# Kernel optimization log

Hardware: AMD Instinct MI355X
Metric: run time of the kernel (lower is better)

## Reference

```python
import jax, jax.numpy as jnp
import numpy as np

N = 100000
E = 625000
IN_C, HID_C, OUT_C = 128, 128, 128


def setup_inputs() -> dict:
    key = jax.random.key(0)
    ks = jax.random.split(key, 8)
    x = jax.random.normal(ks[0], (N, IN_C), dtype=jnp.float32)
    edge_index = jax.random.randint(ks[1], (2, E), 0, N, dtype=jnp.int64)
    # SAGEConv layer 1: lin_l (on aggregated neighbors, with bias), lin_r (on root, no bias)
    s1 = 1.0 / np.sqrt(IN_C)
    W1l = jax.random.uniform(ks[2], (HID_C, IN_C), minval=-s1, maxval=s1, dtype=jnp.float32)
    b1l = jax.random.uniform(ks[3], (HID_C,), minval=-s1, maxval=s1, dtype=jnp.float32)
    W1r = jax.random.uniform(ks[4], (HID_C, IN_C), minval=-s1, maxval=s1, dtype=jnp.float32)
    s2 = 1.0 / np.sqrt(HID_C)
    W2l = jax.random.uniform(ks[5], (OUT_C, HID_C), minval=-s2, maxval=s2, dtype=jnp.float32)
    b2l = jax.random.uniform(ks[6], (OUT_C,), minval=-s2, maxval=s2, dtype=jnp.float32)
    W2r = jax.random.uniform(ks[7], (OUT_C, HID_C), minval=-s2, maxval=s2, dtype=jnp.float32)
    return {"x": x, "edge_index": edge_index,
            "W1l": W1l, "b1l": b1l, "W1r": W1r,
            "W2l": W2l, "b2l": b2l, "W2r": W2r}


def _sage_conv(x, src, dst, Wl, bl, Wr, num_nodes):
    # mean aggregation of source features into destination nodes
    agg = jax.ops.segment_sum(x[src], dst, num_segments=num_nodes)  # [N, d]
    cnt = jax.ops.segment_sum(jnp.ones((src.shape[0],), dtype=x.dtype), dst,
                              num_segments=num_nodes)  # [N]
    mean = agg / jnp.maximum(cnt, 1.0)[:, None]  # zero-degree nodes stay 0
    return mean @ Wl.T + bl + x @ Wr.T


def reference(x, edge_index, W1l, b1l, W1r, W2l, b2l, W2r):
    src, dst = edge_index[0], edge_index[1]
    h = jax.nn.sigmoid(_sage_conv(x, src, dst, W1l, b1l, W1r, N))
    out = _sage_conv(h, src, dst, W2l, b2l, W2r, N)
    return out
```

## Files before the change

kernel.cpp:

```cpp
#include <hip/hip_runtime.h>
#include <math.h>

#define NN 100000
#define NE 625000
#define CC 128
#define CAP 32
#define NT2 1563
#define LSTR 264

typedef __attribute__((ext_vector_type(8))) short bf16x8;
typedef __attribute__((ext_vector_type(4))) float f32x4;

__device__ __forceinline__ unsigned short f2b(float f) {
    unsigned int u = __float_as_uint(f);
    unsigned int r = (u + 0x7FFFu + ((u >> 16) & 1u)) >> 16;
    return (unsigned short)r;
}
__device__ __forceinline__ float b2f(unsigned int h) {
    return __uint_as_float(h << 16);
}


#define PREP_BUILD_B 2442
#define PREP_CVTX_B  12500
#define PREP_CVTW_B  256
#define PREP_TOTAL_B (PREP_BUILD_B + PREP_CVTX_B + PREP_CVTW_B)

__global__ __launch_bounds__(256) void prep_kernel(
        const int* __restrict__ src, const int* __restrict__ dst,
        int* __restrict__ cnt, int* __restrict__ col,
        const float* __restrict__ x, unsigned short* __restrict__ xb,
        const float* __restrict__ W1l, const float* __restrict__ W1r,
        const float* __restrict__ W2l, const float* __restrict__ W2r,
        unsigned short* __restrict__ Wcat1, unsigned short* __restrict__ Wcat2) {
    const int bid = blockIdx.x;
    const int tid = threadIdx.x;

    const int bidx = bid / 6;
    if ((bid % 6) == 0 && bidx < PREP_BUILD_B) {
        int e = bidx * 256 + tid;
        if (e < NE) {
            int d = dst[e];
            int p = atomicAdd(&cnt[d], 1);
            if (p < CAP) col[d * CAP + p] = src[e];
        }
        return;
    }
    int nbuild = (bid + 5) / 6;
    if (nbuild > PREP_BUILD_B) nbuild = PREP_BUILD_B;
    const int cidx = bid - nbuild;
    if (cidx < PREP_CVTX_B) {
        size_t i = ((size_t)cidx * 256 + tid) * 4;
        float4 v = *(const float4*)&x[i];
        uint2 o;
        o.x = (unsigned int)f2b(v.x) | ((unsigned int)f2b(v.y) << 16);
        o.y = (unsigned int)f2b(v.z) | ((unsigned int)f2b(v.w) << 16);
        *(uint2*)&xb[i] = o;
    } else {
        int i = (cidx - PREP_CVTX_B) * 256 + tid;
        int layer = i >> 15;
        int local = i & 32767;
        int c = local >> 8;
        int k = local & 255;
        const float* Wl = layer ? W2l : W1l;
        const float* Wr = layer ? W2r : W1r;
        float v = (k < CC) ? Wl[c * CC + k] : Wr[c * CC + (k - CC)];
        (layer ? Wcat2 : Wcat1)[local] = f2b(v);
    }
}


#define ACC8(u, m) \
    s0 = fmaf(m, b2f((u).x & 0xFFFFu), s0); s1 = fmaf(m, b2f((u).x >> 16), s1); \
    s2 = fmaf(m, b2f((u).y & 0xFFFFu), s2); s3 = fmaf(m, b2f((u).y >> 16), s3); \
    s4 = fmaf(m, b2f((u).z & 0xFFFFu), s4); s5 = fmaf(m, b2f((u).z >> 16), s5); \
    s6 = fmaf(m, b2f((u).w & 0xFFFFu), s6); s7 = fmaf(m, b2f((u).w >> 16), s7);

__global__ __launch_bounds__(256) void gather_kernel(const unsigned short* __restrict__ feat,
                                                     const int* __restrict__ cnt,
                                                     const int* __restrict__ col,
                                                     unsigned short* __restrict__ aggb) {
    int gtid = blockIdx.x * blockDim.x + threadIdx.x;
    int node = gtid >> 4;
    if (node >= NN) return;
    int c8 = (gtid & 15) * 8;
    int deg = cnt[node];
    int dmin = deg < CAP ? deg : CAP;
    const int* __restrict__ bucket = col + node * CAP;
    float s0 = 0, s1 = 0, s2 = 0, s3 = 0, s4 = 0, s5 = 0, s6 = 0, s7 = 0;
    int dpad = (dmin + 7) & ~7;
    for (int j = 0; j < dpad; j += 8) {
        uint4 bA = *(const uint4*)&bucket[j];
        uint4 bB = *(const uint4*)&bucket[j + 4];
        int nfb = (int)bA.x;
        int nb[8] = { (int)bA.x, (int)bA.y, (int)bA.z, (int)bA.w,
                      (int)bB.x, (int)bB.y, (int)bB.z, (int)bB.w };
        int   n[8];
        float msk[8];
        int rem = dmin - j;
#pragma unroll
        for (int q = 0; q < 8; ++q) {
            bool valid = q < rem;
            msk[q] = valid ? 1.0f : 0.0f;
            n[q]   = valid ? nb[q] : nfb;
        }
        uint4 u[8];
#pragma unroll
        for (int q = 0; q < 8; ++q)
            u[q] = *(const uint4*)&feat[(size_t)n[q] * CC + c8];
#pragma unroll
        for (int q = 0; q < 8; ++q) { ACC8(u[q], msk[q]); }
    }
    float iv = 1.0f / (float)(deg > 0 ? deg : 1);
    uint4 o;
    o.x = (unsigned int)f2b(s0 * iv) | ((unsigned int)f2b(s1 * iv) << 16);
    o.y = (unsigned int)f2b(s2 * iv) | ((unsigned int)f2b(s3 * iv) << 16);
    o.z = (unsigned int)f2b(s4 * iv) | ((unsigned int)f2b(s5 * iv) << 16);
    o.w = (unsigned int)f2b(s6 * iv) | ((unsigned int)f2b(s7 * iv) << 16);
    *(uint4*)&aggb[(size_t)node * CC + c8] = o;
}


template<bool SIGMOID, bool OUT_FP32>
__global__ __launch_bounds__(256, 4) void gemm3_kernel(
        const unsigned short* __restrict__ aggb,
        const unsigned short* __restrict__ featb,
        const unsigned short* __restrict__ Wcat,
        const float* __restrict__ bias,
        void* __restrict__ outv) {
    __shared__ unsigned short Acat[64 * LSTR];

    const int t    = threadIdx.x;
    const int w    = t >> 6;
    const int lane = t & 63;
    const int m    = lane & 15;
    const int kq   = lane >> 4;
    const int col0 = w * 32;

    bf16x8 breg[2][8];
#pragma unroll
    for (int ct = 0; ct < 2; ++ct)
#pragma unroll
        for (int ks = 0; ks < 8; ++ks)
            breg[ct][ks] = *(const bf16x8*)(Wcat + (size_t)(col0 + ct * 16 + m) * 256 + ks * 32 + kq * 8);

    const float bias0 = bias[col0 + m];
    const float bias1 = bias[col0 + 16 + m];

    const int sr  = t >> 2;
    const int seg = t & 3;

    for (int rt = blockIdx.x; rt < NT2; rt += gridDim.x) {
        const int row0 = rt * 64;

        int gr = row0 + sr; if (gr >= NN) gr = NN - 1;
        const unsigned short* srcp = (seg < 2)
            ? (aggb  + (size_t)gr * CC + seg * 64)
            : (featb + (size_t)gr * CC + (seg - 2) * 64);
        bf16x8 st[8];
#pragma unroll
        for (int j = 0; j < 8; ++j) st[j] = *(const bf16x8*)(srcp + j * 8);

        __syncthreads();

        unsigned short* q = &Acat[sr * LSTR + seg * 64];
#pragma unroll
        for (int j = 0; j < 8; ++j) *(bf16x8*)(q + j * 8) = st[j];

        __syncthreads();

        f32x4 acc[4][2];
#pragma unroll
        for (int rt4 = 0; rt4 < 4; ++rt4)
#pragma unroll
            for (int ct = 0; ct < 2; ++ct) acc[rt4][ct] = (f32x4)0.0f;

#pragma unroll
        for (int ks = 0; ks < 8; ++ks) {
            bf16x8 a[4];
#pragma unroll
            for (int rt4 = 0; rt4 < 4; ++rt4)
                a[rt4] = *(const bf16x8*)&Acat[(rt4 * 16 + m) * LSTR + ks * 32 + kq * 8];
#pragma unroll
            for (int rt4 = 0; rt4 < 4; ++rt4) {
                acc[rt4][0] = __builtin_amdgcn_mfma_f32_16x16x32_bf16(a[rt4], breg[0][ks], acc[rt4][0], 0, 0, 0);
                acc[rt4][1] = __builtin_amdgcn_mfma_f32_16x16x32_bf16(a[rt4], breg[1][ks], acc[rt4][1], 0, 0, 0);
            }
        }

#pragma unroll
        for (int rt4 = 0; rt4 < 4; ++rt4) {
#pragma unroll
            for (int ct = 0; ct < 2; ++ct) {
                const int c = col0 + ct * 16 + m;
                const float bv = ct ? bias1 : bias0;
#pragma unroll
                for (int i = 0; i < 4; ++i) {
                    const int r = row0 + rt4 * 16 + kq * 4 + i;
                    if (r < NN) {
                        float v = acc[rt4][ct][i] + bv;
                        if (SIGMOID) v = 1.0f / (1.0f + __expf(-v));
                        if (OUT_FP32) __builtin_nontemporal_store(v, &((float*)outv)[(size_t)r * CC + c]);
                        else ((unsigned short*)outv)[(size_t)r * CC + c] = f2b(v);
                    }
                }
            }
        }
    }
}


extern "C" void kernel_launch(void* const* d_in, const int* in_sizes, int n_in,
                              void* d_out, int out_size, void* d_ws, size_t ws_size,
                              hipStream_t stream) {
    const float* x   = (const float*)d_in[0];
    const int*   ei  = (const int*)d_in[1];
    const float* W1l = (const float*)d_in[2];
    const float* b1l = (const float*)d_in[3];
    const float* W1r = (const float*)d_in[4];
    const float* W2l = (const float*)d_in[5];
    const float* b2l = (const float*)d_in[6];
    const float* W2r = (const float*)d_in[7];
    float* out = (float*)d_out;

    const int* src = ei;
    const int* dst = ei + NE;

    int* cnt = (int*)d_ws;
    int* col = cnt + NN;
    unsigned short* Wcat1 = (unsigned short*)(col + NN * CAP);
    unsigned short* Wcat2 = Wcat1 + 128 * 256;
    unsigned short* xb    = Wcat2 + 128 * 256;
    unsigned short* aggb  = xb + (size_t)NN * CC;
    unsigned short* hb    = aggb + (size_t)NN * CC;

    hipMemsetAsync(cnt, 0, (size_t)NN * sizeof(int), stream);

    prep_kernel<<<PREP_TOTAL_B, 256, 0, stream>>>(src, dst, cnt, col, x, xb,
                                                  W1l, W1r, W2l, W2r, Wcat1, Wcat2);

    const int GB = 782;

    gather_kernel<<<(NN * 16) / 256, 256, 0, stream>>>(xb, cnt, col, aggb);
    gemm3_kernel<true, false><<<GB, 256, 0, stream>>>(aggb, xb, Wcat1, b1l, hb);

    gather_kernel<<<(NN * 16) / 256, 256, 0, stream>>>(hb, cnt, col, aggb);
    gemm3_kernel<false, true><<<GB, 256, 0, stream>>>(aggb, hb, Wcat2, b2l, out);
}
```

Before: 255.2 us.

## Fuse all stages into one persistent kernel with global grid barriers

Replaces the five separate kernel launches (prep, two gathers, two GEMMs) with a single persistent kernel that loops over work items and synchronises phases with atomic-counter grid barriers. The grid size comes from an occupancy query, capped at 4 blocks per CU across 256 CUs. This is meant to remove launch overhead and the idle gaps between kernels. In exchange, every block waits at each barrier for the slowest block. The barrier relies on all blocks being co-resident, and it has a spin timeout that could silently break correctness.

```diff
diff --git a/kernel.cpp b/kernel.cpp
--- a/kernel.cpp
+++ b/kernel.cpp
@@ -7,6 +7,12 @@
 #define CAP 32
 #define NT2 1563
 #define LSTR 264
+#define NTH  256
+
+#define PREP_BUILD_B 2442
+#define PREP_CVTX_B  12500
+#define PREP_CVTW_B  256
+#define PREP_TOTAL_B (PREP_BUILD_B + PREP_CVTX_B + PREP_CVTW_B)
 
 typedef __attribute__((ext_vector_type(8))) short bf16x8;
 typedef __attribute__((ext_vector_type(4))) float f32x4;
@@ -21,54 +27,20 @@
 }
 
 
-#define PREP_BUILD_B 2442
-#define PREP_CVTX_B  12500
-#define PREP_CVTW_B  256
-#define PREP_TOTAL_B (PREP_BUILD_B + PREP_CVTX_B + PREP_CVTW_B)
-
-__global__ __launch_bounds__(256) void prep_kernel(
-        const int* __restrict__ src, const int* __restrict__ dst,
-        int* __restrict__ cnt, int* __restrict__ col,
-        const float* __restrict__ x, unsigned short* __restrict__ xb,
-        const float* __restrict__ W1l, const float* __restrict__ W1r,
-        const float* __restrict__ W2l, const float* __restrict__ W2r,
-        unsigned short* __restrict__ Wcat1, unsigned short* __restrict__ Wcat2) {
-    const int bid = blockIdx.x;
-    const int tid = threadIdx.x;
-
-    const int bidx = bid / 6;
-    if ((bid % 6) == 0 && bidx < PREP_BUILD_B) {
-        int e = bidx * 256 + tid;
-        if (e < NE) {
-            int d = dst[e];
-            int p = atomicAdd(&cnt[d], 1);
-            if (p < CAP) col[d * CAP + p] = src[e];
-        }
-        return;
-    }
-    int nbuild = (bid + 5) / 6;
-    if (nbuild > PREP_BUILD_B) nbuild = PREP_BUILD_B;
-    const int cidx = bid - nbuild;
-    if (cidx < PREP_CVTX_B) {
-        size_t i = ((size_t)cidx * 256 + tid) * 4;
-        float4 v = *(const float4*)&x[i];
-        uint2 o;
-        o.x = (unsigned int)f2b(v.x) | ((unsigned int)f2b(v.y) << 16);
-        o.y = (unsigned int)f2b(v.z) | ((unsigned int)f2b(v.w) << 16);
-        *(uint2*)&xb[i] = o;
-    } else {
-        int i = (cidx - PREP_CVTX_B) * 256 + tid;
-        int layer = i >> 15;
-        int local = i & 32767;
-        int c = local >> 8;
-        int k = local & 255;
-        const float* Wl = layer ? W2l : W1l;
-        const float* Wr = layer ? W2r : W1r;
-        float v = (k < CC) ? Wl[c * CC + k] : Wr[c * CC + (k - CC)];
-        (layer ? Wcat2 : Wcat1)[local] = f2b(v);
-    }
-}
-
+__device__ __forceinline__ void gbarrier(unsigned int* __restrict__ bar, int tid) {
+    __syncthreads();
+    if (tid == 0) {
+        __threadfence();
+        atomicAdd(bar, 1u);
+        int spins = 0;
+        while (atomicAdd(bar, 0u) < gridDim.x) {
+            __builtin_amdgcn_s_sleep(2);
+            if (++spins > (1 << 24)) break;
+        }
+        __threadfence();
+    }
+    __syncthreads();
+}
 
 #define ACC8(u, m) \
     s0 = fmaf(m, b2f((u).x & 0xFFFFu), s0); s1 = fmaf(m, b2f((u).x >> 16), s1); \
@@ -76,66 +48,64 @@
     s4 = fmaf(m, b2f((u).z & 0xFFFFu), s4); s5 = fmaf(m, b2f((u).z >> 16), s5); \
     s6 = fmaf(m, b2f((u).w & 0xFFFFu), s6); s7 = fmaf(m, b2f((u).w >> 16), s7);
 
-__global__ __launch_bounds__(256) void gather_kernel(const unsigned short* __restrict__ feat,
-                                                     const int* __restrict__ cnt,
-                                                     const int* __restrict__ col,
-                                                     unsigned short* __restrict__ aggb) {
-    int gtid = blockIdx.x * blockDim.x + threadIdx.x;
-    int node = gtid >> 4;
-    if (node >= NN) return;
-    int c8 = (gtid & 15) * 8;
-    int deg = cnt[node];
-    int dmin = deg < CAP ? deg : CAP;
-    const int* __restrict__ bucket = col + node * CAP;
-    float s0 = 0, s1 = 0, s2 = 0, s3 = 0, s4 = 0, s5 = 0, s6 = 0, s7 = 0;
-    int dpad = (dmin + 7) & ~7;
-    for (int j = 0; j < dpad; j += 8) {
-        uint4 bA = *(const uint4*)&bucket[j];
-        uint4 bB = *(const uint4*)&bucket[j + 4];
-        int nfb = (int)bA.x;
-        int nb[8] = { (int)bA.x, (int)bA.y, (int)bA.z, (int)bA.w,
-                      (int)bB.x, (int)bB.y, (int)bB.z, (int)bB.w };
-        int   n[8];
-        float msk[8];
-        int rem = dmin - j;
-#pragma unroll
-        for (int q = 0; q < 8; ++q) {
-            bool valid = q < rem;
-            msk[q] = valid ? 1.0f : 0.0f;
-            n[q]   = valid ? nb[q] : nfb;
-        }
-        uint4 u[8];
-#pragma unroll
-        for (int q = 0; q < 8; ++q)
-            u[q] = *(const uint4*)&feat[(size_t)n[q] * CC + c8];
-#pragma unroll
-        for (int q = 0; q < 8; ++q) { ACC8(u[q], msk[q]); }
-    }
-    float iv = 1.0f / (float)(deg > 0 ? deg : 1);
-    uint4 o;
-    o.x = (unsigned int)f2b(s0 * iv) | ((unsigned int)f2b(s1 * iv) << 16);
-    o.y = (unsigned int)f2b(s2 * iv) | ((unsigned int)f2b(s3 * iv) << 16);
-    o.z = (unsigned int)f2b(s4 * iv) | ((unsigned int)f2b(s5 * iv) << 16);
-    o.w = (unsigned int)f2b(s6 * iv) | ((unsigned int)f2b(s7 * iv) << 16);
-    *(uint4*)&aggb[(size_t)node * CC + c8] = o;
-}
-
+__device__ __forceinline__ void gather_phase(const unsigned short* __restrict__ feat,
+                                             const int* __restrict__ cnt,
+                                             const int* __restrict__ col,
+                                             unsigned short* __restrict__ aggb,
+                                             int bid, int tid, int nblk) {
+    const int sub = tid >> 4;
+    const int c8  = (tid & 15) * 8;
+    for (int vb = bid; vb < NN / 16; vb += nblk) {
+        const int node = vb * 16 + sub;
+        int deg = cnt[node];
+        int dmin = deg < CAP ? deg : CAP;
+        const int* __restrict__ bucket = col + (size_t)node * CAP;
+        float s0 = 0, s1 = 0, s2 = 0, s3 = 0, s4 = 0, s5 = 0, s6 = 0, s7 = 0;
+        int dpad = (dmin + 7) & ~7;
+        for (int j = 0; j < dpad; j += 8) {
+            uint4 bA = *(const uint4*)&bucket[j];
+            uint4 bB = *(const uint4*)&bucket[j + 4];
+            int nfb = (int)bA.x;
+            int nb[8] = { (int)bA.x, (int)bA.y, (int)bA.z, (int)bA.w,
+                          (int)bB.x, (int)bB.y, (int)bB.z, (int)bB.w };
+            int   n[8];
+            float msk[8];
+            int rem = dmin - j;
+#pragma unroll
+            for (int q = 0; q < 8; ++q) {
+                bool valid = q < rem;
+                msk[q] = valid ? 1.0f : 0.0f;
+                n[q]   = valid ? nb[q] : nfb;
+            }
+            uint4 u[8];
+#pragma unroll
+            for (int q = 0; q < 8; ++q)
+                u[q] = *(const uint4*)&feat[(size_t)n[q] * CC + c8];
+#pragma unroll
+            for (int q = 0; q < 8; ++q) { ACC8(u[q], msk[q]); }
+        }
+        float iv = 1.0f / (float)(deg > 0 ? deg : 1);
+        uint4 o;
+        o.x = (unsigned int)f2b(s0 * iv) | ((unsigned int)f2b(s1 * iv) << 16);
+        o.y = (unsigned int)f2b(s2 * iv) | ((unsigned int)f2b(s3 * iv) << 16);
+        o.z = (unsigned int)f2b(s4 * iv) | ((unsigned int)f2b(s5 * iv) << 16);
+        o.w = (unsigned int)f2b(s6 * iv) | ((unsigned int)f2b(s7 * iv) << 16);
+        *(uint4*)&aggb[(size_t)node * CC + c8] = o;
+    }
+}
 
 template<bool SIGMOID, bool OUT_FP32>
-__global__ __launch_bounds__(256, 4) void gemm3_kernel(
-        const unsigned short* __restrict__ aggb,
-        const unsigned short* __restrict__ featb,
-        const unsigned short* __restrict__ Wcat,
-        const float* __restrict__ bias,
-        void* __restrict__ outv) {
-    __shared__ unsigned short Acat[64 * LSTR];
-
-    const int t    = threadIdx.x;
-    const int w    = t >> 6;
+__device__ __forceinline__ void gemm_phase(unsigned short* __restrict__ Acat,
+                                           const unsigned short* __restrict__ aggb,
+                                           const unsigned short* __restrict__ featb,
+                                           const unsigned short* __restrict__ Wcat,
+                                           const float* __restrict__ bias,
+                                           void* __restrict__ outv,
+                                           int bid, int t, int nblk) {
     const int lane = t & 63;
     const int m    = lane & 15;
     const int kq   = lane >> 4;
-    const int col0 = w * 32;
+    const int col0 = (t >> 6) * 32;
 
     bf16x8 breg[2][8];
 #pragma unroll
@@ -150,7 +120,7 @@
     const int sr  = t >> 2;
     const int seg = t & 3;
 
-    for (int rt = blockIdx.x; rt < NT2; rt += gridDim.x) {
+    for (int rt = bid; rt < NT2; rt += nblk) {
         const int row0 = rt * 64;
 
         int gr = row0 + sr; if (gr >= NN) gr = NN - 1;
@@ -207,6 +177,62 @@
             }
         }
     }
+}
+
+__global__ __launch_bounds__(NTH, 4) void fused_kernel(
+        const int* __restrict__ src, const int* __restrict__ dst,
+        int* __restrict__ cnt, int* __restrict__ col,
+        const float* __restrict__ x, unsigned short* __restrict__ xb,
+        const float* __restrict__ W1l, const float* __restrict__ W1r,
+        const float* __restrict__ W2l, const float* __restrict__ W2r,
+        unsigned short* __restrict__ Wcat1, unsigned short* __restrict__ Wcat2,
+        const float* __restrict__ b1l, const float* __restrict__ b2l,
+        unsigned short* __restrict__ aggb, unsigned short* __restrict__ hb,
+        float* __restrict__ out, unsigned int* __restrict__ bar) {
+    __shared__ unsigned short Acat[64 * LSTR];
+    const int bid  = blockIdx.x;
+    const int tid  = threadIdx.x;
+    const int nblk = gridDim.x;
+
+    for (int c = bid; c < PREP_TOTAL_B; c += nblk) {
+        if (c < PREP_BUILD_B) {
+            int e = c * 256 + tid;
+            if (e < NE) {
+                int d = dst[e];
+                int p = atomicAdd(&cnt[d], 1);
+                if (p < CAP) col[d * CAP + p] = src[e];
+            }
+        } else if (c < PREP_BUILD_B + PREP_CVTX_B) {
+            size_t i = ((size_t)(c - PREP_BUILD_B) * 256 + tid) * 4;
+            float4 v = *(const float4*)&x[i];
+            uint2 o;
+            o.x = (unsigned int)f2b(v.x) | ((unsigned int)f2b(v.y) << 16);
+            o.y = (unsigned int)f2b(v.z) | ((unsigned int)f2b(v.w) << 16);
+            *(uint2*)&xb[i] = o;
+        } else {
+            int i = (c - PREP_BUILD_B - PREP_CVTX_B) * 256 + tid;
+            int layer = i >> 15;
+            int local = i & 32767;
+            int cc = local >> 8;
+            int k  = local & 255;
+            const float* Wl = layer ? W2l : W1l;
+            const float* Wr = layer ? W2r : W1r;
+            float v = (k < CC) ? Wl[cc * CC + k] : Wr[cc * CC + (k - CC)];
+            (layer ? Wcat2 : Wcat1)[local] = f2b(v);
+        }
+    }
+    gbarrier(bar + 0, tid);
+
+    gather_phase(xb, cnt, col, aggb, bid, tid, nblk);
+    gbarrier(bar + 16, tid);
+
+    gemm_phase<true, false>(Acat, aggb, xb, Wcat1, b1l, (void*)hb, bid, tid, nblk);
+    gbarrier(bar + 32, tid);
+
+    gather_phase(hb, cnt, col, aggb, bid, tid, nblk);
+    gbarrier(bar + 48, tid);
+
+    gemm_phase<false, true>(Acat, aggb, hb, Wcat2, b2l, (void*)out, bid, tid, nblk);
 }
 
 
@@ -226,7 +252,8 @@
     const int* src = ei;
     const int* dst = ei + NE;
 
-    int* cnt = (int*)d_ws;
+    unsigned int* bar = (unsigned int*)d_ws;
+    int* cnt = (int*)d_ws + 64;
     int* col = cnt + NN;
     unsigned short* Wcat1 = (unsigned short*)(col + NN * CAP);
     unsigned short* Wcat2 = Wcat1 + 128 * 256;
@@ -234,16 +261,19 @@
     unsigned short* aggb  = xb + (size_t)NN * CC;
     unsigned short* hb    = aggb + (size_t)NN * CC;
 
-    hipMemsetAsync(cnt, 0, (size_t)NN * sizeof(int), stream);
-
-    prep_kernel<<<PREP_TOTAL_B, 256, 0, stream>>>(src, dst, cnt, col, x, xb,
-                                                  W1l, W1r, W2l, W2r, Wcat1, Wcat2);
-
-    const int GB = 782;
-
-    gather_kernel<<<(NN * 16) / 256, 256, 0, stream>>>(xb, cnt, col, aggb);
-    gemm3_kernel<true, false><<<GB, 256, 0, stream>>>(aggb, xb, Wcat1, b1l, hb);
-
-    gather_kernel<<<(NN * 16) / 256, 256, 0, stream>>>(hb, cnt, col, aggb);
-    gemm3_kernel<false, true><<<GB, 256, 0, stream>>>(aggb, hb, Wcat2, b2l, out);
-}
+    hipMemsetAsync(d_ws, 0, (64 + NN) * sizeof(int), stream);
+
+    static int nblk = 0;
+    if (nblk == 0) {
+        int perCU = 0;
+        hipError_t e = hipOccupancyMaxActiveBlocksPerMultiprocessor(
+            &perCU, (const void*)fused_kernel, NTH, 0);
+        if (e != hipSuccess || perCU < 1) perCU = 1;
+        if (perCU > 4) perCU = 4;
+        nblk = perCU * 256;
+    }
+
+    fused_kernel<<<nblk, NTH, 0, stream>>>(src, dst, cnt, col, x, xb,
+                                           W1l, W1r, W2l, W2r, Wcat1, Wcat2,
+                                           b1l, b2l, aggb, hb, out, bar);
+}
```

Measured after the change: 505.4 us. 98.0% more time.
